# Kernel tuning notes

Hardware: AMD Instinct MI355X
Metric: run time of the kernel (lower is better)

Reference implementation:

```python
import jax, jax.numpy as jnp
import numpy as np

N = 100000      # nodes
E = 1600000     # edges
F_IN = 128      # num_features
H = 64          # hidden_channels
EPS = 1e-5      # batchnorm eps


def _bn(x, gamma, beta, mean, var):
    # inference-mode BatchNorm1d
    return (x - mean) * jax.lax.rsqrt(var + EPS) * gamma + beta


def setup_inputs() -> dict:
    key = jax.random.key(0)
    ks = jax.random.split(key, 16)

    def lin_w(k, fan_in, fan_out):
        return (jax.random.normal(k, (fan_in, fan_out), jnp.float32)
                * (1.0 / np.sqrt(fan_in)))

    return {
        "x": jax.random.normal(ks[0], (N, F_IN), jnp.float32),
        "edge_index": jax.random.randint(ks[1], (2, E), 0, N, dtype=jnp.int32),
        # node_encoder: Linear(F_IN,H) + BN
        "enc_W": lin_w(ks[2], F_IN, H), "enc_b": jnp.zeros((H,), jnp.float32),
        "enc_g": jnp.ones((H,), jnp.float32), "enc_beta": jnp.zeros((H,), jnp.float32),
        "enc_mean": jnp.zeros((H,), jnp.float32), "enc_var": jnp.ones((H,), jnp.float32),
        # GCNConv layers (PyG: lin without bias, bias added after aggregation)
        "conv1_W": lin_w(ks[3], H, H), "conv1_b": jnp.zeros((H,), jnp.float32),
        "conv2_W": lin_w(ks[4], H, H), "conv2_b": jnp.zeros((H,), jnp.float32),
        # edge_predictor: Linear(2H,H) + BN + Linear(H,1)
        "ep1_W": lin_w(ks[5], 2 * H, H), "ep1_b": jnp.zeros((H,), jnp.float32),
        "ep_g": jnp.ones((H,), jnp.float32), "ep_beta": jnp.zeros((H,), jnp.float32),
        "ep_mean": jnp.zeros((H,), jnp.float32), "ep_var": jnp.ones((H,), jnp.float32),
        "ep2_W": lin_w(ks[6], H, 1), "ep2_b": jnp.zeros((1,), jnp.float32),
    }


def reference(x, edge_index, enc_W, enc_b, enc_g, enc_beta, enc_mean, enc_var,
              conv1_W, conv1_b, conv2_W, conv2_b,
              ep1_W, ep1_b, ep_g, ep_beta, ep_mean, ep_var, ep2_W, ep2_b):
    row, col = edge_index[0], edge_index[1]

    # GCN normalization with added self-loops (symmetric D^-1/2 (A+I) D^-1/2)
    loops = jnp.arange(N, dtype=row.dtype)
    row_sl = jnp.concatenate([row, loops])          # [E+N]
    col_sl = jnp.concatenate([col, loops])
    deg = jax.ops.segment_sum(jnp.ones_like(col_sl, jnp.float32), col_sl, N)
    dinv = jnp.where(deg > 0, jax.lax.rsqrt(jnp.maximum(deg, 1.0)), 0.0)
    norm = dinv[row_sl] * dinv[col_sl]              # [E+N]

    def gcn_conv(h, W, b):
        hw = h @ W                                   # [N,H]
        msg = hw[row_sl] * norm[:, None]             # gather-scale  [E+N,H]
        return jax.ops.segment_sum(msg, col_sl, N) + b  # scatter-add

    # node encoder (inference: dropout = identity)
    h = jax.nn.relu(_bn(x @ enc_W + enc_b, enc_g, enc_beta, enc_mean, enc_var))
    h = jax.nn.relu(gcn_conv(h, conv1_W, conv1_b))
    h = jax.nn.relu(gcn_conv(h, conv2_W, conv2_b))
    node_embeddings = h

    # edge predictor: gather + cat + MLP + sigmoid
    ef = jnp.concatenate([h[row], h[col]], axis=1)   # [E, 2H]
    e = jax.nn.relu(_bn(ef @ ep1_W + ep1_b, ep_g, ep_beta, ep_mean, ep_var))
    edge_pred = jax.nn.sigmoid(e @ ep2_W + ep2_b)    # [E, 1]
    return node_embeddings, edge_pred
```

## Files before the change

### kernel.cpp

```cpp
#include <hip/hip_runtime.h>
#include <hip/hip_bf16.h>
#include <hip/hip_fp16.h>

#define NN 100000
#define NE 1600000
#define FIN 128
#define HD 64
#define NB_MF 1563
#define BSH 8
#define BUCK 256
#define NBUCK 392
#define BCAP 5120
#define CHUNK 4096
#define NCHUNK 391
#define ESPLIT 2
#define NEB (NBUCK*ESPLIT)
#define NFB 6250
#define NAGG 6250

typedef unsigned int uint32;
typedef _Float16 half8 __attribute__((ext_vector_type(8)));
typedef float f32x4 __attribute__((ext_vector_type(4)));
typedef float f32x8 __attribute__((ext_vector_type(8)));

__global__ void __launch_bounds__(256) k_pp(const int* __restrict__ row,
                                            const int* __restrict__ col,
                                            int* __restrict__ bcnt,
                                            uint32* __restrict__ staged,
                                            uint32* __restrict__ posE,
                                            const float* __restrict__ encW, const float* __restrict__ c1W,
                                            const float* __restrict__ c2W, const float* __restrict__ ep1W,
                                            _Float16* __restrict__ wt,
                                            const float* __restrict__ encB, const float* __restrict__ encG,
                                            const float* __restrict__ encBe, const float* __restrict__ encM,
                                            const float* __restrict__ encV,
                                            const float* __restrict__ ep1b, const float* __restrict__ epG,
                                            const float* __restrict__ epBe, const float* __restrict__ epM,
                                            const float* __restrict__ epV,
                                            float* __restrict__ foldEnc, float* __restrict__ foldPre,
                                            _Float16* __restrict__ bufBzero){
    int blk = blockIdx.x, t = threadIdx.x;
    if(blk < NCHUNK){
        __shared__ int h[512];
        __shared__ int sc[512];
        __shared__ int gb[512];
        __shared__ uint32 lcsr[CHUNK];
        __shared__ int dst[CHUNK];
        int e0 = blk * CHUNK;
        int e1 = min(e0 + CHUNK, NE);
        h[t] = 0; h[256+t] = 0;
        __syncthreads();
        for(int e = e0 + t; e < e1; e += 256)
            atomicAdd(&h[col[e] >> BSH], 1);
        __syncthreads();
        int c0 = h[t], c1 = h[256+t];
        int i2 = 256 + t;
        gb[t]  = (c0 > 0) ? atomicAdd(&bcnt[t], c0) : 0;
        gb[i2] = (i2 < NBUCK && c1 > 0) ? atomicAdd(&bcnt[i2], c1) : 0;
        sc[t] = c0; __syncthreads();
        for(int off = 1; off < 256; off <<= 1){
            int a = (t >= off) ? sc[t-off] : 0;
            __syncthreads();
            sc[t] += a;
            __syncthreads();
        }
        int sum0 = sc[255];
        __syncthreads();
        sc[i2] = c1; __syncthreads();
        for(int off = 1; off < 256; off <<= 1){
            int a = (t >= off) ? sc[i2-off] : 0;
            __syncthreads();
            sc[i2] += a;
            __syncthreads();
        }
        __syncthreads();
        {
            int st0 = sc[t] - c0;
            int st1 = sc[i2] + sum0 - c1;
            h[t]   = st0;
            h[i2]  = st1;
            sc[t]  = t*BCAP  + gb[t]  - st0;
            sc[i2] = i2*BCAP + gb[i2] - st1;
        }
        __syncthreads();
        for(int e = e0 + t; e < e1; e += 256){
            int c = col[e], r = row[e];
            int b = c >> BSH;
            int p = atomicAdd(&h[b], 1);
            lcsr[p] = ((uint32)r << BSH) | (uint32)(c & (BUCK-1));
            int slot = sc[b] + p;
            int off  = slot - b*BCAP;
            bool ok  = (off < BCAP);
            dst[p]   = ok ? slot : -1;
            posE[e]  = ok ? (uint32)slot : 0xFFFFFFFFu;
        }
        __syncthreads();
        int cnt = e1 - e0;
        for(int i = t; i < cnt; i += 256){
            int d = dst[i];
            if(d >= 0) staged[d] = lcsr[i];
        }
    } else {
        int pblk = blk - NCHUNK;
        if(pblk < 96){
            int i = pblk*256 + t;
            if(i < 8192){
                int n = i >> 7, k = i & 127;
                wt[i] = (_Float16)encW[k*64 + n];
            } else if(i < 12288){
                int j = i - 8192; int n = j >> 6, k = j & 63;
                wt[i] = (_Float16)c1W[k*64 + n];
            } else if(i < 16384){
                int j = i - 12288; int n = j >> 6, k = j & 63;
                wt[i] = (_Float16)c2W[k*64 + n];
            } else {
                int j = i - 16384; int hh = j >> 12; int jj = j & 4095;
                int n = jj >> 6, k = jj & 63;
                wt[i] = (_Float16)ep1W[(hh*64 + k)*64 + n];
            }
        } else {
            if(t < 64){
                int j = t;
                float s = encG[j]*rsqrtf(encV[j]+1e-5f);
                foldEnc[j]      = s;
                foldEnc[64+j]   = (encB[j]-encM[j])*s + encBe[j];
                float sp = epG[j]*rsqrtf(epV[j]+1e-5f);
                foldPre[j]      = sp;
                foldPre[64+j]   = sp;
                foldPre[128+j]  = sp*(ep1b[j]-epM[j]) + epBe[j];
                foldPre[192+j]  = 0.f;
                bufBzero[j]     = (_Float16)0.f;
            }
        }
    }
}

__global__ void __launch_bounds__(256) k_fe(const int* __restrict__ bcnt,
                                            const uint32* __restrict__ staged,
                                            int* __restrict__ deg,
                                            int* __restrict__ starts,
                                            float* __restrict__ dinv,
                                            int* __restrict__ csr,
                                            const float* __restrict__ x,
                                            const _Float16* __restrict__ wt,
                                            const float* __restrict__ foldEnc,
                                            _Float16* __restrict__ bufA){
    __shared__ union U {
        struct { int h[BUCK]; int sc[BUCK]; int red[256]; int lcsr[BCAP]; } f;
        struct { _Float16 As[64*136]; _Float16 Bs[64*136]; } m;
    } sh;
    int blk = blockIdx.x, t = threadIdx.x;
    if(blk < NBUCK){
        int b = blk;
        int part = 0;
        for(int i = t; i < b; i += 256) part += min(bcnt[i], BCAP);
        sh.f.red[t] = part; __syncthreads();
        for(int off = 128; off > 0; off >>= 1){
            if(t < off) sh.f.red[t] += sh.f.red[t+off];
            __syncthreads();
        }
        int base = sh.f.red[0];
        sh.f.h[t] = 0;
        __syncthreads();
        int cnt = min(bcnt[b], BCAP);
        const uint32* st = staged + (size_t)b*BCAP;
        for(int i = t; i < cnt; i += 256) atomicAdd(&sh.f.h[st[i] & (BUCK-1)], 1);
        __syncthreads();
        int v = sh.f.h[t];
        sh.f.sc[t] = v; __syncthreads();
        for(int off = 1; off < 256; off <<= 1){
            int a = (t >= off) ? sh.f.sc[t-off] : 0;
            __syncthreads();
            sh.f.sc[t] += a;
            __syncthreads();
        }
        int ex = sh.f.sc[t] - v;
        int n = b*BUCK + t;
        if(n < NN){
            deg[n]    = v;
            starts[n] = base + ex;
            dinv[n]   = rsqrtf((float)(v + 1));
        }
        sh.f.h[t] = ex;
        __syncthreads();
        for(int i = t; i < cnt; i += 256){
            uint32 u = st[i];
            int p = atomicAdd(&sh.f.h[u & (BUCK-1)], 1);
            sh.f.lcsr[p] = (int)(u >> BSH);
        }
        __syncthreads();
        for(int i = t; i < cnt; i += 256) csr[base + i] = sh.f.lcsr[i];
    } else {
        constexpr int K = FIN, PS = K + 8;
        int m0 = (blk - NBUCK)*64;
        for(int idx = t; idx < 64*(K/8); idx += 256){
            int n = idx/(K/8), c = idx%(K/8);
            *(half8*)&sh.m.Bs[n*PS + c*8] = *(const half8*)&wt[n*K + c*8];
        }
        for(int idx = t; idx < 64*(K/4); idx += 256){
            int r = idx/(K/4), c = idx%(K/4);
            int rowi = m0 + r; if(rowi >= NN) rowi = NN-1;
            float4 v = *(const float4*)&x[(size_t)rowi*K + c*4];
            _Float16* d = &sh.m.As[r*PS + c*4];
            d[0]=(_Float16)v.x; d[1]=(_Float16)v.y; d[2]=(_Float16)v.z; d[3]=(_Float16)v.w;
        }
        __syncthreads();
        int w = t>>6, l = t&63;
        int lm = l&15, q = l>>4;
        f32x4 acc0 = {0.f,0.f,0.f,0.f}, acc1 = {0.f,0.f,0.f,0.f};
        f32x4 acc2 = {0.f,0.f,0.f,0.f}, acc3 = {0.f,0.f,0.f,0.f};
        const _Float16* arow = &sh.m.As[(w*16+lm)*PS + q*8];
        const _Float16* brow = &sh.m.Bs[lm*PS + q*8];
        #pragma unroll
        for(int ks = 0; ks < K/32; ks++){
            half8 a  = *(const half8*)(arow + ks*32);
            half8 b0 = *(const half8*)(brow + ks*32);
            half8 b1 = *(const half8*)(brow + 16*PS + ks*32);
            half8 b2 = *(const half8*)(brow + 32*PS + ks*32);
            half8 b3 = *(const half8*)(brow + 48*PS + ks*32);
            acc0 = __builtin_amdgcn_mfma_f32_16x16x32_f16(a, b0, acc0, 0,0,0);
            acc1 = __builtin_amdgcn_mfma_f32_16x16x32_f16(a, b1, acc1, 0,0,0);
            acc2 = __builtin_amdgcn_mfma_f32_16x16x32_f16(a, b2, acc2, 0,0,0);
            acc3 = __builtin_amdgcn_mfma_f32_16x16x32_f16(a, b3, acc3, 0,0,0);
        }
        f32x4 accs[4] = {acc0, acc1, acc2, acc3};
        #pragma unroll
        for(int nt = 0; nt < 4; nt++){
            int jcol = nt*16 + lm;
            float fs = foldEnc[jcol];
            float fb = foldEnc[64 + jcol];
            #pragma unroll
            for(int r = 0; r < 4; r++){
                int rowi = m0 + w*16 + q*4 + r;
                if(rowi >= NN) continue;
                float v = accs[nt][r]*fs + fb;
                v = fmaxf(v, 0.f);
                bufA[(size_t)rowi*64 + jcol] = (_Float16)v;
            }
        }
    }
}

template<int K, bool AF32, bool FOLD, bool RELU, bool SCALE, int OS>
__global__ void __launch_bounds__(256) k_mfma(const void* __restrict__ Ain,
                                              const _Float16* __restrict__ Bt,
                                              const float* __restrict__ fold,
                                              const float* __restrict__ rowscale,
                                              _Float16* __restrict__ outh){
    constexpr int PS = K + 8;
    __shared__ _Float16 As[64*PS];
    __shared__ _Float16 Bs[64*PS];
    int t = threadIdx.x;
    int m0 = blockIdx.x*64;
    int jh = blockIdx.y;
    {
        const _Float16* src = Bt + (size_t)jh*64*K;
        for(int idx = t; idx < 64*(K/8); idx += 256){
            int n = idx/(K/8), c = idx%(K/8);
            *(half8*)&Bs[n*PS + c*8] = *(const half8*)&src[n*K + c*8];
        }
    }
    if(AF32){
        const float* A = (const float*)Ain;
        for(int idx = t; idx < 64*(K/4); idx += 256){
            int r = idx/(K/4), c = idx%(K/4);
            int rowi = m0 + r; if(rowi >= NN) rowi = NN-1;
            float4 v = *(const float4*)&A[(size_t)rowi*K + c*4];
            _Float16* d = &As[r*PS + c*4];
            d[0]=(_Float16)v.x; d[1]=(_Float16)v.y; d[2]=(_Float16)v.z; d[3]=(_Float16)v.w;
        }
    } else {
        const _Float16* A = (const _Float16*)Ain;
        for(int idx = t; idx < 64*(K/8); idx += 256){
            int r = idx/(K/8), c = idx%(K/8);
            int rowi = m0 + r; if(rowi >= NN) rowi = NN-1;
            *(half8*)&As[r*PS + c*8] = *(const half8*)&A[(size_t)rowi*K + c*8];
        }
    }
    __syncthreads();
    int w = t>>6, l = t&63;
    int lm = l&15, q = l>>4;
    f32x4 acc0 = {0.f,0.f,0.f,0.f}, acc1 = {0.f,0.f,0.f,0.f};
    f32x4 acc2 = {0.f,0.f,0.f,0.f}, acc3 = {0.f,0.f,0.f,0.f};
    const _Float16* arow = &As[(w*16+lm)*PS + q*8];
    const _Float16* brow = &Bs[lm*PS + q*8];
    #pragma unroll
    for(int ks = 0; ks < K/32; ks++){
        half8 a  = *(const half8*)(arow + ks*32);
        half8 b0 = *(const half8*)(brow + ks*32);
        half8 b1 = *(const half8*)(brow + 16*PS + ks*32);
        half8 b2 = *(const half8*)(brow + 32*PS + ks*32);
        half8 b3 = *(const half8*)(brow + 48*PS + ks*32);
        acc0 = __builtin_amdgcn_mfma_f32_16x16x32_f16(a, b0, acc0, 0,0,0);
        acc1 = __builtin_amdgcn_mfma_f32_16x16x32_f16(a, b1, acc1, 0,0,0);
        acc2 = __builtin_amdgcn_mfma_f32_16x16x32_f16(a, b2, acc2, 0,0,0);
        acc3 = __builtin_amdgcn_mfma_f32_16x16x32_f16(a, b3, acc3, 0,0,0);
    }
    f32x4 accs[4] = {acc0, acc1, acc2, acc3};
    #pragma unroll
    for(int nt = 0; nt < 4; nt++){
        int col = nt*16 + lm;
        int jcol = jh*64 + col;
        float fs = FOLD ? fold[jcol] : 0.f;
        float fb = FOLD ? fold[OS + jcol] : 0.f;
        #pragma unroll
        for(int r = 0; r < 4; r++){
            int rowi = m0 + w*16 + q*4 + r;
            if(rowi >= NN) continue;
            float v = accs[nt][r];
            if(FOLD) v = v*fs + fb;
            if(RELU) v = fmaxf(v, 0.f);
            if(SCALE) v *= rowscale[rowi];
            outh[(size_t)rowi*OS + jcol] = (_Float16)v;
        }
    }
}

__global__ void __launch_bounds__(256) k_agg4(const _Float16* __restrict__ hb,
                                              const int* __restrict__ starts,
                                              const int* __restrict__ deg,
                                              const int* __restrict__ csr,
                                              const float* __restrict__ dinv,
                                              const float* __restrict__ bias,
                                              _Float16* __restrict__ outh,
                                              float* __restrict__ outf){
    int t = threadIdx.x, w = t>>6, f = t&63;
    int n0 = blockIdx.x*16 + w*4;
    int s0 = __builtin_amdgcn_readfirstlane(starts[n0+0]);
    int s1 = __builtin_amdgcn_readfirstlane(starts[n0+1]);
    int s2 = __builtin_amdgcn_readfirstlane(starts[n0+2]);
    int s3 = __builtin_amdgcn_readfirstlane(starts[n0+3]);
    int d0 = __builtin_amdgcn_readfirstlane(deg[n0+0]);
    int d1 = __builtin_amdgcn_readfirstlane(deg[n0+1]);
    int d2 = __builtin_amdgcn_readfirstlane(deg[n0+2]);
    int d3 = __builtin_amdgcn_readfirstlane(deg[n0+3]);
    float a0 = 0.f, a1 = 0.f, a2 = 0.f, a3 = 0.f;
    int dmax = max(max(d0,d1), max(d2,d3));
    for(int i0 = 0; i0 < dmax; i0 += 64){
        int li0 = (i0+f < d0) ? csr[s0+i0+f] : NN;
        int li1 = (i0+f < d1) ? csr[s1+i0+f] : NN;
        int li2 = (i0+f < d2) ? csr[s2+i0+f] : NN;
        int li3 = (i0+f < d3) ? csr[s3+i0+f] : NN;
        int mm = min(dmax - i0, 64);
        for(int j = 0; j < mm; j += 8){
            float t0 = 0.f, t1 = 0.f, t2 = 0.f, t3 = 0.f;
            #pragma unroll
            for(int u = 0; u < 8; u++){
                int r0 = __builtin_amdgcn_readlane(li0, j+u);
                int r1 = __builtin_amdgcn_readlane(li1, j+u);
                int r2 = __builtin_amdgcn_readlane(li2, j+u);
                int r3 = __builtin_amdgcn_readlane(li3, j+u);
                t0 += (float)hb[(size_t)r0*64 + f];
                t1 += (float)hb[(size_t)r1*64 + f];
                t2 += (float)hb[(size_t)r2*64 + f];
                t3 += (float)hb[(size_t)r3*64 + f];
            }
            a0 += t0; a1 += t1; a2 += t2; a3 += t3;
        }
    }
    float bv = bias[f];
    float dn0 = dinv[n0+0], dn1 = dinv[n0+1], dn2 = dinv[n0+2], dn3 = dinv[n0+3];
    float sf0 = (float)hb[(size_t)(n0+0)*64 + f];
    float sf1 = (float)hb[(size_t)(n0+1)*64 + f];
    float sf2 = (float)hb[(size_t)(n0+2)*64 + f];
    float sf3 = (float)hb[(size_t)(n0+3)*64 + f];
    float o0 = fmaxf((a0 + sf0)*dn0 + bv, 0.f);
    float o1 = fmaxf((a1 + sf1)*dn1 + bv, 0.f);
    float o2 = fmaxf((a2 + sf2)*dn2 + bv, 0.f);
    float o3 = fmaxf((a3 + sf3)*dn3 + bv, 0.f);
    outh[(size_t)(n0+0)*64 + f] = (_Float16)o0;
    outh[(size_t)(n0+1)*64 + f] = (_Float16)o1;
    outh[(size_t)(n0+2)*64 + f] = (_Float16)o2;
    outh[(size_t)(n0+3)*64 + f] = (_Float16)o3;
    if(outf){
        outf[(size_t)(n0+0)*64 + f] = o0;
        outf[(size_t)(n0+1)*64 + f] = o1;
        outf[(size_t)(n0+2)*64 + f] = o2;
        outf[(size_t)(n0+3)*64 + f] = o3;
    }
}

__global__ void __launch_bounds__(512) k_edgeb(const int* __restrict__ bcnt,
                                               const uint32* __restrict__ staged,
                                               const _Float16* __restrict__ pre,
                                               const float* __restrict__ w2,
                                               const float* __restrict__ b2,
                                               _Float16* __restrict__ zqh){
    __shared__ half8 Bl[BUCK*8];
    int t = threadIdx.x;
    int item = ((int)blockIdx.x & 7)*98 + ((int)blockIdx.x >> 3);
    int b = item >> 1, s = item & 1;
    const _Float16* ps = pre;
    for(int idx = t; idx < BUCK*8; idx += 512){
        int rl = idx >> 3, ch = idx & 7;
        int n = (b << BSH) + rl; if(n >= NN) n = NN-1;
        Bl[rl*8 + (ch ^ (rl & 7))] = *(const half8*)(ps + (size_t)n*128 + 64 + ch*8);
    }
    __syncthreads();

    int cnt = min(bcnt[b], BCAP);
    int lo = (cnt * s) >> 1, hi = (cnt * (s+1)) >> 1;
    const uint32* st = staged + (size_t)b*BCAP;
    _Float16* zb = zqh + (size_t)b*BCAP;
    int p  = t & 7;
    int oc = t >> 3;
    f32x8 w2v = *(const f32x8*)(w2 + 8*p);
    float b2v = b2[0];

    auto edot = [&](uint32 u)->float{
        int r  = (int)(u >> BSH);
        int cl = (int)(u & (BUCK-1));
        half8 av = *(const half8*)(ps + (size_t)r*128 + 8*p);
        half8 bv = Bl[cl*8 + (p ^ (cl & 7))];
        half8 sv = av + bv;
        half8 zero8 = {};
        half8 rv = __builtin_elementwise_max(sv, zero8);
        f32x8 fv = __builtin_convertvector(rv, f32x8);
        float z;
        z  = fv[0]*w2v[0] + fv[1]*w2v[1];
        z  = fmaf(fv[2], w2v[2], z); z = fmaf(fv[3], w2v[3], z);
        z  = fmaf(fv[4], w2v[4], z); z = fmaf(fv[5], w2v[5], z);
        z  = fmaf(fv[6], w2v[6], z); z = fmaf(fv[7], w2v[7], z);
        return z;
    };

    int i = lo + oc;
    for(; i + 64 < hi; i += 128){
        uint32 u0 = st[i], u1 = st[i+64];
        float z0 = edot(u0);
        float z1 = edot(u1);
        z0 += __shfl_xor(z0, 1, 64); z1 += __shfl_xor(z1, 1, 64);
        z0 += __shfl_xor(z0, 2, 64); z1 += __shfl_xor(z1, 2, 64);
        z0 += __shfl_xor(z0, 4, 64); z1 += __shfl_xor(z1, 4, 64);
        if(p == 0){
            zb[i]    = (_Float16)(1.f/(1.f+__expf(-(z0+b2v))));
            zb[i+64] = (_Float16)(1.f/(1.f+__expf(-(z1+b2v))));
        }
    }
    for(; i < hi; i += 64){
        uint32 u0 = st[i];
        float z0 = edot(u0);
        z0 += __shfl_xor(z0, 1, 64);
        z0 += __shfl_xor(z0, 2, 64);
        z0 += __shfl_xor(z0, 4, 64);
        if(p == 0) zb[i] = (_Float16)(1.f/(1.f+__expf(-(z0+b2v))));
    }
}

__global__ void __launch_bounds__(256) k_final(const uint32* __restrict__ posE,
                                               const _Float16* __restrict__ zqh,
                                               float* __restrict__ out){
    int e = blockIdx.x*256 + threadIdx.x;
    if(e < NE){
        uint32 pz = posE[e];
        out[e] = (float)zqh[pz < (uint32)(NBUCK*BCAP) ? pz : 0u];
    }
}


extern "C" void kernel_launch(void* const* d_in, const int* in_sizes, int n_in,
                              void* d_out, int out_size, void* d_ws, size_t ws_size,
                              hipStream_t stream){
    const float* x   = (const float*)d_in[0];
    const int* ei    = (const int*)d_in[1];
    const int* row   = ei;
    const int* col   = ei + NE;
    const float* encW = (const float*)d_in[2],  *encB = (const float*)d_in[3];
    const float* encG = (const float*)d_in[4],  *encBe= (const float*)d_in[5];
    const float* encM = (const float*)d_in[6],  *encV = (const float*)d_in[7];
    const float* c1W  = (const float*)d_in[8],  *c1b  = (const float*)d_in[9];
    const float* c2W  = (const float*)d_in[10], *c2b  = (const float*)d_in[11];
    const float* ep1W = (const float*)d_in[12], *ep1b = (const float*)d_in[13];
    const float* epG  = (const float*)d_in[14], *epBe = (const float*)d_in[15];
    const float* epM  = (const float*)d_in[16], *epV  = (const float*)d_in[17];
    const float* ep2W = (const float*)d_in[18], *ep2b = (const float*)d_in[19];

    char* wsc = (char*)d_ws;
    size_t o = 0;
    auto alloc = [&](size_t bytes)->void*{
        void* p = wsc + o; o += (bytes + 255) & ~(size_t)255; return p;
    };
    int*      deg     = (int*)     alloc((size_t)NN*4);
    int*      starts  = (int*)     alloc((size_t)NN*4);
    int*      bcnt    = (int*)     alloc((size_t)NBUCK*4);
    int*      csr     = (int*)     alloc((size_t)NE*4);
    uint32*   staged  = (uint32*)  alloc((size_t)NBUCK*BCAP*4);
    float*    dinv    = (float*)   alloc((size_t)NN*4);
    float*    foldEnc = (float*)   alloc(128*4);
    float*    foldPre = (float*)   alloc(256*4);
    _Float16* wt      = (_Float16*)alloc(24576*2);
    _Float16* bufA    = (_Float16*)alloc((size_t)NN*64*2);
    _Float16* bufB    = (_Float16*)alloc((size_t)(NN+1)*64*2);
    _Float16* preh    = (_Float16*)alloc((size_t)NN*128*2);
    uint32*   posE    = (uint32*)  alloc((size_t)NE*4);
    _Float16* zqh     = (_Float16*)alloc((size_t)NBUCK*BCAP*2);

    float* outp = (float*)d_out;
    float* node_out = outp;
    float* edge_out = outp + (size_t)NN*64;

    hipMemsetAsync(bcnt, 0, (size_t)NBUCK*4, stream);
    k_pp <<<NCHUNK + 97, 256, 0, stream>>>(row, col, bcnt, staged, posE,
                                           encW, c1W, c2W, ep1W, wt,
                                           encB, encG, encBe, encM, encV,
                                           ep1b, epG, epBe, epM, epV,
                                           foldEnc, foldPre, bufB + (size_t)NN*64);
    k_fe <<<NBUCK + NB_MF, 256, 0, stream>>>(bcnt, staged, deg, starts, dinv, csr,
                                             x, wt, foldEnc, bufA);

    k_mfma<64,false,false,false,true,64><<<dim3(NB_MF,1), 256, 0, stream>>>
        (bufA, wt + 8192, nullptr, dinv, bufB);
    k_agg4 <<<NAGG, 256, 0, stream>>>(bufB, starts, deg, csr, dinv, c1b,
                                      bufA, nullptr);

    k_mfma<64,false,false,false,true,64><<<dim3(NB_MF,1), 256, 0, stream>>>
        (bufA, wt + 12288, nullptr, dinv, bufB);
    k_agg4 <<<NAGG, 256, 0, stream>>>(bufB, starts, deg, csr, dinv, c2b,
                                      bufA, node_out);

    k_mfma<64,false,true,false,false,128><<<dim3(NB_MF,2), 256, 0, stream>>>
        (bufA, wt + 16384, foldPre, nullptr, preh);

    k_edgeb<<<NEB, 512, 0, stream>>>(bcnt, staged, (const _Float16*)preh, ep2W, ep2b, zqh);
    k_final<<<NFB, 256, 0, stream>>>(posE, zqh, edge_out);
}
```

Before: 319.2 us.

## Fuse GCN aggregation with the following dense matmul in one kernel

The neighbour-aggregation kernel now also runs the next layer's weight multiply. It writes each 64-row block of aggregated features into LDS and then does MFMA against the next weight matrix, so the intermediate activation no longer round-trips through global memory and two launches are removed. The first conv's matmul becomes a specialised kernel, and a second ping-pong buffer with its own zero pad row is added. The trade-off is fewer aggregation blocks (64 rows per block instead of 16), which lowers the parallelism available to hide the latency of the irregular gathers, plus more LDS per block.

After: 355.7 us. 1.11x slower.

```diff
diff --git a/kernel.cpp b/kernel.cpp
--- a/kernel.cpp
+++ b/kernel.cpp
@@ -16,7 +16,6 @@
 #define ESPLIT 2
 #define NEB (NBUCK*ESPLIT)
 #define NFB 6250
-#define NAGG 6250
 
 typedef unsigned int uint32;
 typedef _Float16 half8 __attribute__((ext_vector_type(8)));
@@ -38,7 +37,8 @@
                                             const float* __restrict__ epBe, const float* __restrict__ epM,
                                             const float* __restrict__ epV,
                                             float* __restrict__ foldEnc, float* __restrict__ foldPre,
-                                            _Float16* __restrict__ bufBzero){
+                                            _Float16* __restrict__ bufBzero,
+                                            _Float16* __restrict__ bufB2zero){
     int blk = blockIdx.x, t = threadIdx.x;
     if(blk < NCHUNK){
         __shared__ int h[512];
@@ -130,6 +130,7 @@
                 foldPre[128+j]  = sp*(ep1b[j]-epM[j]) + epBe[j];
                 foldPre[192+j]  = 0.f;
                 bufBzero[j]     = (_Float16)0.f;
+                bufB2zero[j]    = (_Float16)0.f;
             }
         }
     }
@@ -241,41 +242,23 @@
     }
 }
 
-template<int K, bool AF32, bool FOLD, bool RELU, bool SCALE, int OS>
-__global__ void __launch_bounds__(256) k_mfma(const void* __restrict__ Ain,
+__global__ void __launch_bounds__(256) k_mfc1(const _Float16* __restrict__ A,
                                               const _Float16* __restrict__ Bt,
-                                              const float* __restrict__ fold,
                                               const float* __restrict__ rowscale,
                                               _Float16* __restrict__ outh){
-    constexpr int PS = K + 8;
+    constexpr int K = 64, PS = K + 8;
     __shared__ _Float16 As[64*PS];
     __shared__ _Float16 Bs[64*PS];
     int t = threadIdx.x;
     int m0 = blockIdx.x*64;
-    int jh = blockIdx.y;
-    {
-        const _Float16* src = Bt + (size_t)jh*64*K;
-        for(int idx = t; idx < 64*(K/8); idx += 256){
-            int n = idx/(K/8), c = idx%(K/8);
-            *(half8*)&Bs[n*PS + c*8] = *(const half8*)&src[n*K + c*8];
-        }
-    }
-    if(AF32){
-        const float* A = (const float*)Ain;
-        for(int idx = t; idx < 64*(K/4); idx += 256){
-            int r = idx/(K/4), c = idx%(K/4);
-            int rowi = m0 + r; if(rowi >= NN) rowi = NN-1;
-            float4 v = *(const float4*)&A[(size_t)rowi*K + c*4];
-            _Float16* d = &As[r*PS + c*4];
-            d[0]=(_Float16)v.x; d[1]=(_Float16)v.y; d[2]=(_Float16)v.z; d[3]=(_Float16)v.w;
-        }
-    } else {
-        const _Float16* A = (const _Float16*)Ain;
-        for(int idx = t; idx < 64*(K/8); idx += 256){
-            int r = idx/(K/8), c = idx%(K/8);
-            int rowi = m0 + r; if(rowi >= NN) rowi = NN-1;
-            *(half8*)&As[r*PS + c*8] = *(const half8*)&A[(size_t)rowi*K + c*8];
-        }
+    for(int idx = t; idx < 64*(K/8); idx += 256){
+        int n = idx/(K/8), c = idx%(K/8);
+        *(half8*)&Bs[n*PS + c*8] = *(const half8*)&Bt[n*K + c*8];
+    }
+    for(int idx = t; idx < 64*(K/8); idx += 256){
+        int r = idx/(K/8), c = idx%(K/8);
+        int rowi = m0 + r; if(rowi >= NN) rowi = NN-1;
+        *(half8*)&As[r*PS + c*8] = *(const half8*)&A[(size_t)rowi*K + c*8];
     }
     __syncthreads();
     int w = t>>6, l = t&63;
@@ -299,84 +282,131 @@
     f32x4 accs[4] = {acc0, acc1, acc2, acc3};
     #pragma unroll
     for(int nt = 0; nt < 4; nt++){
-        int col = nt*16 + lm;
-        int jcol = jh*64 + col;
-        float fs = FOLD ? fold[jcol] : 0.f;
-        float fb = FOLD ? fold[OS + jcol] : 0.f;
+        int jcol = nt*16 + lm;
         #pragma unroll
         for(int r = 0; r < 4; r++){
             int rowi = m0 + w*16 + q*4 + r;
             if(rowi >= NN) continue;
-            float v = accs[nt][r];
-            if(FOLD) v = v*fs + fb;
-            if(RELU) v = fmaxf(v, 0.f);
-            if(SCALE) v *= rowscale[rowi];
-            outh[(size_t)rowi*OS + jcol] = (_Float16)v;
-        }
-    }
-}
-
-__global__ void __launch_bounds__(256) k_agg4(const _Float16* __restrict__ hb,
-                                              const int* __restrict__ starts,
-                                              const int* __restrict__ deg,
-                                              const int* __restrict__ csr,
-                                              const float* __restrict__ dinv,
-                                              const float* __restrict__ bias,
-                                              _Float16* __restrict__ outh,
-                                              float* __restrict__ outf){
+            float v = accs[nt][r] * rowscale[rowi];
+            outh[(size_t)rowi*64 + jcol] = (_Float16)v;
+        }
+    }
+}
+
+template<int NJH, bool SCALE, bool FOLD, bool WRITEF>
+__global__ void __launch_bounds__(256) k_aggmm(const _Float16* __restrict__ hb,
+                                               const int* __restrict__ starts,
+                                               const int* __restrict__ deg,
+                                               const int* __restrict__ csr,
+                                               const float* __restrict__ dinv,
+                                               const float* __restrict__ bias,
+                                               const _Float16* __restrict__ Bt,
+                                               const float* __restrict__ fold,
+                                               float* __restrict__ outf,
+                                               _Float16* __restrict__ outh){
+    constexpr int K = 64, PS = K + 8;
+    __shared__ _Float16 As[64*PS];
+    __shared__ _Float16 Bs[NJH*64*PS];
     int t = threadIdx.x, w = t>>6, f = t&63;
-    int n0 = blockIdx.x*16 + w*4;
-    int s0 = __builtin_amdgcn_readfirstlane(starts[n0+0]);
-    int s1 = __builtin_amdgcn_readfirstlane(starts[n0+1]);
-    int s2 = __builtin_amdgcn_readfirstlane(starts[n0+2]);
-    int s3 = __builtin_amdgcn_readfirstlane(starts[n0+3]);
-    int d0 = __builtin_amdgcn_readfirstlane(deg[n0+0]);
-    int d1 = __builtin_amdgcn_readfirstlane(deg[n0+1]);
-    int d2 = __builtin_amdgcn_readfirstlane(deg[n0+2]);
-    int d3 = __builtin_amdgcn_readfirstlane(deg[n0+3]);
-    float a0 = 0.f, a1 = 0.f, a2 = 0.f, a3 = 0.f;
-    int dmax = max(max(d0,d1), max(d2,d3));
-    for(int i0 = 0; i0 < dmax; i0 += 64){
-        int li0 = (i0+f < d0) ? csr[s0+i0+f] : NN;
-        int li1 = (i0+f < d1) ? csr[s1+i0+f] : NN;
-        int li2 = (i0+f < d2) ? csr[s2+i0+f] : NN;
-        int li3 = (i0+f < d3) ? csr[s3+i0+f] : NN;
-        int mm = min(dmax - i0, 64);
-        for(int j = 0; j < mm; j += 8){
-            float t0 = 0.f, t1 = 0.f, t2 = 0.f, t3 = 0.f;
+    int m0 = blockIdx.x*64;
+    for(int idx = t; idx < NJH*64*8; idx += 256){
+        int n = idx>>3, c = idx&7;
+        *(half8*)&Bs[n*PS + c*8] = *(const half8*)&Bt[n*K + c*8];
+    }
+    float bv = bias[f];
+    for(int g = 0; g < 4; g++){
+        int rb = w*16 + g*4;
+        int na = min(m0+rb+0, NN-1), nb = min(m0+rb+1, NN-1);
+        int nc = min(m0+rb+2, NN-1), nd = min(m0+rb+3, NN-1);
+        int s0 = __builtin_amdgcn_readfirstlane(starts[na]);
+        int s1 = __builtin_amdgcn_readfirstlane(starts[nb]);
+        int s2 = __builtin_amdgcn_readfirstlane(starts[nc]);
+        int s3 = __builtin_amdgcn_readfirstlane(starts[nd]);
+        int d0 = __builtin_amdgcn_readfirstlane(deg[na]);
+        int d1 = __builtin_amdgcn_readfirstlane(deg[nb]);
+        int d2 = __builtin_amdgcn_readfirstlane(deg[nc]);
+        int d3 = __builtin_amdgcn_readfirstlane(deg[nd]);
+        float a0 = 0.f, a1 = 0.f, a2 = 0.f, a3 = 0.f;
+        int dmax = max(max(d0,d1), max(d2,d3));
+        for(int i0 = 0; i0 < dmax; i0 += 64){
+            int li0 = (i0+f < d0) ? csr[s0+i0+f] : NN;
+            int li1 = (i0+f < d1) ? csr[s1+i0+f] : NN;
+            int li2 = (i0+f < d2) ? csr[s2+i0+f] : NN;
+            int li3 = (i0+f < d3) ? csr[s3+i0+f] : NN;
+            int mm = min(dmax - i0, 64);
+            for(int j = 0; j < mm; j += 8){
+                float t0 = 0.f, t1 = 0.f, t2 = 0.f, t3 = 0.f;
+                #pragma unroll
+                for(int u = 0; u < 8; u++){
+                    int r0 = __builtin_amdgcn_readlane(li0, j+u);
+                    int r1 = __builtin_amdgcn_readlane(li1, j+u);
+                    int r2 = __builtin_amdgcn_readlane(li2, j+u);
+                    int r3 = __builtin_amdgcn_readlane(li3, j+u);
+                    t0 += (float)hb[(size_t)r0*64 + f];
+                    t1 += (float)hb[(size_t)r1*64 + f];
+                    t2 += (float)hb[(size_t)r2*64 + f];
+                    t3 += (float)hb[(size_t)r3*64 + f];
+                }
+                a0 += t0; a1 += t1; a2 += t2; a3 += t3;
+            }
+        }
+        float dn0 = dinv[na], dn1 = dinv[nb], dn2 = dinv[nc], dn3 = dinv[nd];
+        float sf0 = (float)hb[(size_t)na*64 + f];
+        float sf1 = (float)hb[(size_t)nb*64 + f];
+        float sf2 = (float)hb[(size_t)nc*64 + f];
+        float sf3 = (float)hb[(size_t)nd*64 + f];
+        float o0 = fmaxf((a0 + sf0)*dn0 + bv, 0.f);
+        float o1 = fmaxf((a1 + sf1)*dn1 + bv, 0.f);
+        float o2 = fmaxf((a2 + sf2)*dn2 + bv, 0.f);
+        float o3 = fmaxf((a3 + sf3)*dn3 + bv, 0.f);
+        As[(rb+0)*PS + f] = (_Float16)o0;
+        As[(rb+1)*PS + f] = (_Float16)o1;
+        As[(rb+2)*PS + f] = (_Float16)o2;
+        As[(rb+3)*PS + f] = (_Float16)o3;
+        if(WRITEF){
+            if(m0+rb+0 < NN) outf[(size_t)(m0+rb+0)*64 + f] = o0;
+            if(m0+rb+1 < NN) outf[(size_t)(m0+rb+1)*64 + f] = o1;
+            if(m0+rb+2 < NN) outf[(size_t)(m0+rb+2)*64 + f] = o2;
+            if(m0+rb+3 < NN) outf[(size_t)(m0+rb+3)*64 + f] = o3;
+        }
+    }
+    __syncthreads();
+    int l = t&63, lm = l&15, q = l>>4;
+    f32x4 acc[NJH][4] = {};
+    const _Float16* arow = &As[(w*16+lm)*PS + q*8];
+    #pragma unroll
+    for(int ks = 0; ks < 2; ks++){
+        half8 a = *(const half8*)(arow + ks*32);
+        #pragma unroll
+        for(int h = 0; h < NJH; h++){
+            const _Float16* brow = &Bs[h*64*PS + lm*PS + q*8] + ks*32;
+            half8 b0 = *(const half8*)(brow);
+            half8 b1 = *(const half8*)(brow + 16*PS);
+            half8 b2 = *(const half8*)(brow + 32*PS);
+            half8 b3 = *(const half8*)(brow + 48*PS);
+            acc[h][0] = __builtin_amdgcn_mfma_f32_16x16x32_f16(a, b0, acc[h][0], 0,0,0);
+            acc[h][1] = __builtin_amdgcn_mfma_f32_16x16x32_f16(a, b1, acc[h][1], 0,0,0);
+            acc[h][2] = __builtin_amdgcn_mfma_f32_16x16x32_f16(a, b2, acc[h][2], 0,0,0);
+            acc[h][3] = __builtin_amdgcn_mfma_f32_16x16x32_f16(a, b3, acc[h][3], 0,0,0);
+        }
+    }
+    #pragma unroll
+    for(int h = 0; h < NJH; h++){
+        #pragma unroll
+        for(int nt = 0; nt < 4; nt++){
+            int jcol = h*64 + nt*16 + lm;
+            float fs = FOLD ? fold[jcol] : 0.f;
+            float fb = FOLD ? fold[NJH*64 + jcol] : 0.f;
             #pragma unroll
-            for(int u = 0; u < 8; u++){
-                int r0 = __builtin_amdgcn_readlane(li0, j+u);
-                int r1 = __builtin_amdgcn_readlane(li1, j+u);
-                int r2 = __builtin_amdgcn_readlane(li2, j+u);
-                int r3 = __builtin_amdgcn_readlane(li3, j+u);
-                t0 += (float)hb[(size_t)r0*64 + f];
-                t1 += (float)hb[(size_t)r1*64 + f];
-                t2 += (float)hb[(size_t)r2*64 + f];
-                t3 += (float)hb[(size_t)r3*64 + f];
+            for(int r = 0; r < 4; r++){
+                int rowi = m0 + w*16 + q*4 + r;
+                if(rowi >= NN) continue;
+                float v = acc[h][nt][r];
+                if(FOLD) v = v*fs + fb;
+                if(SCALE) v *= dinv[rowi];
+                outh[(size_t)rowi*(NJH*64) + jcol] = (_Float16)v;
             }
-            a0 += t0; a1 += t1; a2 += t2; a3 += t3;
-        }
-    }
-    float bv = bias[f];
-    float dn0 = dinv[n0+0], dn1 = dinv[n0+1], dn2 = dinv[n0+2], dn3 = dinv[n0+3];
-    float sf0 = (float)hb[(size_t)(n0+0)*64 + f];
-    float sf1 = (float)hb[(size_t)(n0+1)*64 + f];
-    float sf2 = (float)hb[(size_t)(n0+2)*64 + f];
-    float sf3 = (float)hb[(size_t)(n0+3)*64 + f];
-    float o0 = fmaxf((a0 + sf0)*dn0 + bv, 0.f);
-    float o1 = fmaxf((a1 + sf1)*dn1 + bv, 0.f);
-    float o2 = fmaxf((a2 + sf2)*dn2 + bv, 0.f);
-    float o3 = fmaxf((a3 + sf3)*dn3 + bv, 0.f);
-    outh[(size_t)(n0+0)*64 + f] = (_Float16)o0;
-    outh[(size_t)(n0+1)*64 + f] = (_Float16)o1;
-    outh[(size_t)(n0+2)*64 + f] = (_Float16)o2;
-    outh[(size_t)(n0+3)*64 + f] = (_Float16)o3;
-    if(outf){
-        outf[(size_t)(n0+0)*64 + f] = o0;
-        outf[(size_t)(n0+1)*64 + f] = o1;
-        outf[(size_t)(n0+2)*64 + f] = o2;
-        outf[(size_t)(n0+3)*64 + f] = o3;
+        }
     }
 }
 
@@ -491,6 +521,7 @@
     _Float16* wt      = (_Float16*)alloc(24576*2);
     _Float16* bufA    = (_Float16*)alloc((size_t)NN*64*2);
     _Float16* bufB    = (_Float16*)alloc((size_t)(NN+1)*64*2);
+    _Float16* bufB2   = (_Float16*)alloc((size_t)(NN+1)*64*2);
     _Float16* preh    = (_Float16*)alloc((size_t)NN*128*2);
     uint32*   posE    = (uint32*)  alloc((size_t)NE*4);
     _Float16* zqh     = (_Float16*)alloc((size_t)NBUCK*BCAP*2);
@@ -504,22 +535,18 @@
                                            encW, c1W, c2W, ep1W, wt,
                                            encB, encG, encBe, encM, encV,
                                            ep1b, epG, epBe, epM, epV,
-                                           foldEnc, foldPre, bufB + (size_t)NN*64);
+                                           foldEnc, foldPre,
+                                           bufB + (size_t)NN*64, bufB2 + (size_t)NN*64);
     k_fe <<<NBUCK + NB_MF, 256, 0, stream>>>(bcnt, staged, deg, starts, dinv, csr,
                                              x, wt, foldEnc, bufA);
 
-    k_mfma<64,false,false,false,true,64><<<dim3(NB_MF,1), 256, 0, stream>>>
-        (bufA, wt + 8192, nullptr, dinv, bufB);
-    k_agg4 <<<NAGG, 256, 0, stream>>>(bufB, starts, deg, csr, dinv, c1b,
-                                      bufA, nullptr);
-
-    k_mfma<64,false,false,false,true,64><<<dim3(NB_MF,1), 256, 0, stream>>>
-        (bufA, wt + 12288, nullptr, dinv, bufB);
-    k_agg4 <<<NAGG, 256, 0, stream>>>(bufB, starts, deg, csr, dinv, c2b,
-                                      bufA, node_out);
-
-    k_mfma<64,false,true,false,false,128><<<dim3(NB_MF,2), 256, 0, stream>>>
-        (bufA, wt + 16384, foldPre, nullptr, preh);
+    k_mfc1<<<NB_MF, 256, 0, stream>>>(bufA, wt + 8192, dinv, bufB);
+
+    k_aggmm<1,true,false,false><<<NB_MF, 256, 0, stream>>>
+        (bufB, starts, deg, csr, dinv, c1b, wt + 12288, nullptr, nullptr, bufB2);
+
+    k_aggmm<2,false,true,true><<<NB_MF, 256, 0, stream>>>
+        (bufB2, starts, deg, csr, dinv, c2b, wt + 16384, foldPre, node_out, preh);
 
     k_edgeb<<<NEB, 512, 0, stream>>>(bcnt, staged, (const _Float16*)preh, ep2W, ep2b, zqh);
     k_final<<<NFB, 256, 0, stream>>>(posE, zqh, edge_out);
```
